# Performance work log

Hardware: AMD Instinct MI355X
Metric: run time of the kernel (lower is better)

## Reference

```python
import jax, jax.numpy as jnp
import numpy as np

K = 7            # pool_size / PSROI_BINS
FEAT_STRIDE = 4
SAMPLES = 2      # bilinear sampling points per bin side (RoIAlign-style avg)


def setup_inputs() -> dict:
    key = jax.random.key(0)
    ks = jax.random.split(key, 4)
    B, H, W, C = 1, 200, 304, 4 * K * K  # C = k*k*dim, dim=4
    features = jax.random.normal(ks[0], (B, H, W, C), jnp.float32)
    Himg, Wimg = H * FEAT_STRIDE, W * FEAT_STRIDE
    N = 512
    u = jax.random.uniform(ks[1], (N, 4), jnp.float32)
    x1 = u[:, 0] * (Wimg - 64.0)
    y1 = u[:, 1] * (Himg - 64.0)
    x2 = jnp.minimum(x1 + 32.0 + u[:, 2] * (Wimg / 4.0), Wimg - 1.0)
    y2 = jnp.minimum(y1 + 32.0 + u[:, 3] * (Himg / 4.0), Himg - 1.0)
    rois = jnp.stack([x1, y1, x2, y2], axis=-1)  # (N,4) image coords
    W_off = jax.random.normal(ks[2], (3, 3, C, 2 * C), jnp.float32) * 0.01
    b_off = jnp.zeros((2 * C,), jnp.float32)
    return {"features": features, "rois": rois, "W_off": W_off, "b_off": b_off}


def _deform_sample(x, off):
    # x: (B,H,W,C); off: (B,H,W,C,2) as (dy,dx) per channel.
    B, H, W, C = x.shape
    gy = jnp.arange(H, dtype=x.dtype)[None, :, None, None]
    gx = jnp.arange(W, dtype=x.dtype)[None, None, :, None]
    yy = jnp.clip(gy + off[..., 0], 0.0, H - 1.0)
    xx = jnp.clip(gx + off[..., 1], 0.0, W - 1.0)
    y0 = jnp.floor(yy); x0 = jnp.floor(xx)
    wy = yy - y0; wx = xx - x0
    y0i = y0.astype(jnp.int32); x0i = x0.astype(jnp.int32)
    y1i = jnp.minimum(y0i + 1, H - 1); x1i = jnp.minimum(x0i + 1, W - 1)
    bi = jnp.arange(B)[:, None, None, None]
    ci = jnp.arange(C)[None, None, None, :]
    v00 = x[bi, y0i, x0i, ci]; v01 = x[bi, y0i, x1i, ci]
    v10 = x[bi, y1i, x0i, ci]; v11 = x[bi, y1i, x1i, ci]
    top = v00 + (v01 - v00) * wx
    bot = v10 + (v11 - v10) * wx
    return top + (bot - top) * wy


def _ps_roi(fm, rois):
    # fm: (H,W,C) offset feature map; rois: (N,4) image coords (x1,y1,x2,y2).
    H, W, C = fm.shape
    dim = C // (K * K)
    fmg = fm.reshape(H, W, K * K, dim)  # position-sensitive channel groups
    b = rois / jnp.asarray(FEAT_STRIDE, fm.dtype)
    x1, y1, x2, y2 = b[:, 0], b[:, 1], b[:, 2], b[:, 3]
    bh = (y2 - y1) / K; bw = (x2 - x1) / K  # per-roi bin sizes (N,)
    i = jnp.arange(K, dtype=fm.dtype)
    s = (jnp.arange(SAMPLES, dtype=fm.dtype) + 0.5) / SAMPLES
    sy = y1[:, None, None] + (i[None, :, None] + s[None, None, :]) * bh[:, None, None]
    sx = x1[:, None, None] + (i[None, :, None] + s[None, None, :]) * bw[:, None, None]
    yy = jnp.clip(sy, 0.0, H - 1.0)[:, :, None, :, None]  # (N,Ki,1,S,1)
    xx = jnp.clip(sx, 0.0, W - 1.0)[:, None, :, None, :]  # (N,1,Kj,1,S)
    y0 = jnp.floor(yy); wy = (yy - y0)[..., None]
    x0 = jnp.floor(xx); wx = (xx - x0)[..., None]
    y0i = y0.astype(jnp.int32); y1i = jnp.minimum(y0i + 1, H - 1)
    x0i = x0.astype(jnp.int32); x1i = jnp.minimum(x0i + 1, W - 1)
    g = (jnp.arange(K)[:, None] * K + jnp.arange(K)[None, :])[None, :, :, None, None]
    v00 = fmg[y0i, x0i, g, :]; v01 = fmg[y0i, x1i, g, :]  # (N,K,K,S,S,dim)
    v10 = fmg[y1i, x0i, g, :]; v11 = fmg[y1i, x1i, g, :]
    top = v00 + (v01 - v00) * wx
    bot = v10 + (v11 - v10) * wx
    vals = top + (bot - top) * wy
    return vals.mean(axis=(3, 4))  # (N,K,K,dim)


def reference(features, rois, W_off, b_off):
    B, H, W, C = features.shape
    offs = jax.lax.conv_general_dilated(
        features, W_off, (1, 1), "SAME",
        dimension_numbers=("NHWC", "HWIO", "NHWC")) + b_off  # (B,H,W,2C)
    off = offs.reshape(B, H, W, C, 2)
    offset_map = _deform_sample(features, off)  # deformable offset resampling
    return _ps_roi(offset_map[0], rois)
```

## Files before the change

kernel.cpp:

```cpp
#include <hip/hip_runtime.h>


constexpr int H = 200, W = 304, C = 196, CO = 392;
constexpr int KK = 7, DIM = 4, NROI = 512;
constexpr int KP = 232;
constexpr int KW = 224;
constexpr size_t WS_NEED = (size_t)49 * 9 * 8 * KW * 2;

typedef __attribute__((ext_vector_type(8))) short bf16x8;
typedef __attribute__((ext_vector_type(4))) float f32x4;

static __device__ inline unsigned short f2bf(float x) {
  unsigned int u = __float_as_uint(x);
  return (unsigned short)((u + 0x7FFFu + ((u >> 16) & 1u)) >> 16);
}

static __device__ inline void roi_geom(const float* __restrict__ rois, int n,
                                       int bi, int bj,
                                       int* ycand, int* xcand,
                                       float* wy, float* wx) {
  const float rx1 = rois[n * 4 + 0] * 0.25f;
  const float ry1 = rois[n * 4 + 1] * 0.25f;
  const float rx2 = rois[n * 4 + 2] * 0.25f;
  const float ry2 = rois[n * 4 + 3] * 0.25f;
  const float bh = (ry2 - ry1) * (1.0f / 7.0f);
  const float bw = (rx2 - rx1) * (1.0f / 7.0f);
#pragma unroll
  for (int si = 0; si < 2; ++si) {
    float sy = ry1 + ((float)bi + ((float)si + 0.5f) * 0.5f) * bh;
    sy = fminf(fmaxf(sy, 0.0f), (float)(H - 1));
    float fy = floorf(sy);
    wy[si] = sy - fy;
    int i0 = (int)fy;
    ycand[2 * si] = i0;
    ycand[2 * si + 1] = min(i0 + 1, H - 1);

    float sx = rx1 + ((float)bj + ((float)si + 0.5f) * 0.5f) * bw;
    sx = fminf(fmaxf(sx, 0.0f), (float)(W - 1));
    float fx = floorf(sx);
    wx[si] = sx - fx;
    int j0 = (int)fx;
    xcand[2 * si] = j0;
    xcand[2 * si + 1] = min(j0 + 1, W - 1);
  }
}

__global__ __launch_bounds__(256) void wprep_kernel(
    const float* __restrict__ Woff, unsigned short* __restrict__ wsb)
{
  const int u = blockIdx.x * 256 + threadIdx.x;
  const int TOT = 49 * 9 * 8 * (KW / 4);
  if (u >= TOT) return;
  const int k4 = u % (KW / 4);
  const int n  = (u / (KW / 4)) % 8;
  const int p  = (u / (KW / 4 * 8)) % 9;
  const int g  = u / (KW / 4 * 8 * 9);
  const int k  = k4 * 4;
  ushort4 v = make_ushort4(0, 0, 0, 0);
  const int o = g * 8 + n;
#pragma unroll
  for (int j = 0; j < 4; ++j) {
    if (k + j < C) {
      const float w = Woff[(size_t)(p * C + k + j) * CO + o];
      ((unsigned short*)&v)[j] = f2bf(w);
    }
  }
  *reinterpret_cast<ushort4*>(wsb + ((size_t)(g * 9 + p) * 8 + n) * KW + k) = v;
}

template <bool USE_WS>
__global__ __launch_bounds__(256) void psroi_union_kernel(
    const float* __restrict__ feat, const float* __restrict__ rois,
    const unsigned short* __restrict__ wsb, const float* __restrict__ Woff,
    const float* __restrict__ boff, float* __restrict__ out)
{
  const int bid = blockIdx.x;
  const int wid = (bid & 7) * (49 * NROI / 8) + (bid >> 3);
  const int g = wid % 49;
  const int n = wid / 49;
  const int bi = g / KK, bj = g % KK;
  const int tid = threadIdx.x;
  const int lane = tid & 63;
  const int wv = tid >> 6;
  const int m_lane = lane & 15;
  const int k_hi = lane >> 4;

  __shared__ short Abuf[64 * KP];
  __shared__ float Cbuf[4 * 16 * 9];

  for (int i = tid; i < 64 * (KP - C); i += 256) {
    const int row = i / (KP - C), col = C + i % (KP - C);
    Abuf[row * KP + col] = 0;
  }

  int yc4[4], xc4[4];
  float wy2[2], wx2[2];
  roi_geom(rois, n, bi, bj, yc4, xc4, wy2, wx2);

  {
    const int pos = tid >> 2;
    const int yi = pos >> 3, xi = pos & 7;
    const int yrow = (yi < 4) ? (yc4[0] + yi - 1) : (yc4[2] + yi - 5);
    const int xcol = (xi < 4) ? (xc4[0] + xi - 1) : (xc4[2] + xi - 5);
    const bool valid = (yrow >= 0) && (yrow < H) && (xcol >= 0) && (xcol < W);
    const float* frow = feat + (size_t)(yrow * W + xcol) * C;
    short* arow = &Abuf[pos * KP];
    const int l = tid & 3;
#pragma unroll
    for (int k = 0; k <= 12; ++k) {
      const int c = l + 4 * k;
      if (c < 49) {
        ushort4 v = make_ushort4(0, 0, 0, 0);
        if (valid) {
          const float4 f4 = *reinterpret_cast<const float4*>(frow + 4 * c);
          v.x = f2bf(f4.x); v.y = f2bf(f4.y);
          v.z = f2bf(f4.z); v.w = f2bf(f4.w);
        }
        *reinterpret_cast<ushort4*>(arow + 4 * c) = v;
      }
    }
  }
  __syncthreads();

  const int i0 = m_lane >> 2, j0 = m_lane & 3;
  const int dyA = yc4[1] - yc4[0], dyB = yc4[3] - yc4[2];
  const int dxA = xc4[1] - xc4[0], dxB = xc4[3] - xc4[2];
  int ybase = (i0 & 2) ? 5 : 1;
  ybase += (i0 & 1) ? ((i0 & 2) ? dyB : dyA) : 0;
  int xbase = (j0 & 2) ? 5 : 1;
  xbase += (j0 & 1) ? ((j0 & 2) ? dxB : dxA) : 0;

  f32x4 acc = {0.f, 0.f, 0.f, 0.f};

#pragma unroll 1
  for (int p = wv; p < 9; p += 4) {
    bf16x8 bfr[7];
#pragma unroll
    for (int ks = 0; ks < 7; ++ks) bfr[ks] = (bf16x8)(short)0;
    if (m_lane < 8) {
      if (USE_WS) {
        const unsigned short* wrow =
            wsb + ((size_t)(g * 9 + p) * 8 + m_lane) * KW + k_hi * 8;
#pragma unroll
        for (int ks = 0; ks < 7; ++ks)
          bfr[ks] = *reinterpret_cast<const bf16x8*>(wrow + ks * 32);
      } else {
#pragma unroll
        for (int ks = 0; ks < 7; ++ks) {
          bf16x8 b = (bf16x8)(short)0;
#pragma unroll
          for (int j = 0; j < 8; ++j) {
            const int k = ks * 32 + k_hi * 8 + j;
            if (k < C)
              b[j] = (short)f2bf(Woff[(size_t)(p * C + k) * CO + g * 8 + m_lane]);
          }
          bfr[ks] = b;
        }
      }
    }

    const int row = (ybase + p / 3 - 1) * 8 + (xbase + p % 3 - 1);
    const short* arow = &Abuf[row * KP];
#pragma unroll
    for (int ks = 0; ks < 7; ++ks) {
      const bf16x8 a = *reinterpret_cast<const bf16x8*>(arow + ks * 32 + k_hi * 8);
      acc = __builtin_amdgcn_mfma_f32_16x16x32_bf16(a, bfr[ks], acc, 0, 0, 0);
    }
  }

  if (m_lane < 8) {
#pragma unroll
    for (int r = 0; r < 4; ++r)
      Cbuf[(wv * 16 + k_hi * 4 + r) * 9 + m_lane] = acc[r];
  }
  __syncthreads();

  if (tid < 64) {
    const int corner = tid >> 2;
    const int d = tid & 3;
    const int yc = yc4[corner >> 2];
    const int xc = xc4[corner & 3];
    const int c = g * DIM + d;

    float offy = boff[2 * c], offx = boff[2 * c + 1];
#pragma unroll
    for (int w = 0; w < 4; ++w) {
      offy += Cbuf[(w * 16 + corner) * 9 + 2 * d];
      offx += Cbuf[(w * 16 + corner) * 9 + 2 * d + 1];
    }

    float yy = fminf(fmaxf((float)yc + offy, 0.0f), (float)(H - 1));
    float xx = fminf(fmaxf((float)xc + offx, 0.0f), (float)(W - 1));
    const float fy = floorf(yy), fx = floorf(xx);
    const float ay = yy - fy, ax = xx - fx;
    const int iy0 = (int)fy, ix0 = (int)fx;
    const int iy1 = min(iy0 + 1, H - 1), ix1 = min(ix0 + 1, W - 1);
    const float v00 = feat[(size_t)(iy0 * W + ix0) * C + c];
    const float v01 = feat[(size_t)(iy0 * W + ix1) * C + c];
    const float v10 = feat[(size_t)(iy1 * W + ix0) * C + c];
    const float v11 = feat[(size_t)(iy1 * W + ix1) * C + c];
    const float top = v00 + (v01 - v00) * ax;
    const float bot = v10 + (v11 - v10) * ax;
    const float om = top + (bot - top) * ay;

    const int yci = corner >> 2, xci = corner & 3;
    const int si = yci >> 1, a = yci & 1;
    const int sj = xci >> 1, b = xci & 1;
    const float cy = a ? wy2[si] : 1.0f - wy2[si];
    const float cx = b ? wx2[sj] : 1.0f - wx2[sj];
    float v = 0.25f * cy * cx * om;

    v += __shfl_xor(v, 4);
    v += __shfl_xor(v, 8);
    v += __shfl_xor(v, 16);
    v += __shfl_xor(v, 32);

    if (tid < 4)
      out[(size_t)n * (KK * KK * DIM) + g * DIM + tid] = v;
  }
}

extern "C" void kernel_launch(void* const* d_in, const int* in_sizes, int n_in,
                              void* d_out, int out_size, void* d_ws, size_t ws_size,
                              hipStream_t stream) {
  const float* feat = (const float*)d_in[0];
  const float* rois = (const float*)d_in[1];
  const float* Woff = (const float*)d_in[2];
  const float* boff = (const float*)d_in[3];
  float* out = (float*)d_out;
  unsigned short* wsb = (unsigned short*)d_ws;

  const int nblocks = 49 * NROI;
  if (ws_size >= WS_NEED) {
    const int prep_tot = 49 * 9 * 8 * (KW / 4);
    wprep_kernel<<<dim3((prep_tot + 255) / 256), dim3(256), 0, stream>>>(Woff, wsb);
    psroi_union_kernel<true><<<dim3(nblocks), dim3(256), 0, stream>>>(
        feat, rois, wsb, Woff, boff, out);
  } else {
    psroi_union_kernel<false><<<dim3(nblocks), dim3(256), 0, stream>>>(
        feat, rois, wsb, Woff, boff, out);
  }
}
```

Before: 208.8 us.

## Pre-convert feature map to padded bf16 and compute one site per wave

Adds a prep kernel that converts the whole feature map to a channel-padded bf16 copy in workspace. A new direct kernel then has each wave handle one (roi, bin) site, loading MFMA A and B operands straight from global bf16 buffers. This removes the per-block LDS staging, fp32-to-bf16 conversion and reduction across waves, and cuts the block count by four. In exchange it needs a much larger workspace and adds a full-map conversion pass; the old kernel stays as the fallback when workspace is too small.

```diff
diff --git a/kernel.cpp b/kernel.cpp
--- a/kernel.cpp
+++ b/kernel.cpp
@@ -3,9 +3,11 @@
 
 constexpr int H = 200, W = 304, C = 196, CO = 392;
 constexpr int KK = 7, DIM = 4, NROI = 512;
+constexpr int KW = 224;
 constexpr int KP = 232;
-constexpr int KW = 224;
-constexpr size_t WS_NEED = (size_t)49 * 9 * 8 * KW * 2;
+constexpr size_t F_ELEMS = (size_t)H * W * KW;
+constexpr size_t W_ELEMS = (size_t)49 * 9 * 8 * KW;
+constexpr size_t WS_NEED = (F_ELEMS + W_ELEMS) * 2;
 
 typedef __attribute__((ext_vector_type(8))) short bf16x8;
 typedef __attribute__((ext_vector_type(4))) float f32x4;
@@ -45,8 +47,25 @@
   }
 }
 
+__global__ __launch_bounds__(256) void fprep_kernel(
+    const float* __restrict__ feat, unsigned short* __restrict__ fbf)
+{
+  const long long u = (long long)blockIdx.x * 256 + threadIdx.x;
+  const long long TOT = (long long)H * W * (KW / 4);
+  if (u >= TOT) return;
+  const int k4 = (int)(u % (KW / 4));
+  const long long pix = u / (KW / 4);
+  const int k = k4 * 4;
+  ushort4 v = make_ushort4(0, 0, 0, 0);
+  const float* src = feat + pix * C;
+#pragma unroll
+  for (int j = 0; j < 4; ++j)
+    if (k + j < C) ((unsigned short*)&v)[j] = f2bf(src[k + j]);
+  *reinterpret_cast<ushort4*>(fbf + pix * KW + k) = v;
+}
+
 __global__ __launch_bounds__(256) void wprep_kernel(
-    const float* __restrict__ Woff, unsigned short* __restrict__ wsb)
+    const float* __restrict__ Woff, unsigned short* __restrict__ wbf)
 {
   const int u = blockIdx.x * 256 + threadIdx.x;
   const int TOT = 49 * 9 * 8 * (KW / 4);
@@ -59,135 +78,74 @@
   ushort4 v = make_ushort4(0, 0, 0, 0);
   const int o = g * 8 + n;
 #pragma unroll
-  for (int j = 0; j < 4; ++j) {
-    if (k + j < C) {
-      const float w = Woff[(size_t)(p * C + k + j) * CO + o];
-      ((unsigned short*)&v)[j] = f2bf(w);
-    }
-  }
-  *reinterpret_cast<ushort4*>(wsb + ((size_t)(g * 9 + p) * 8 + n) * KW + k) = v;
-}
-
-template <bool USE_WS>
-__global__ __launch_bounds__(256) void psroi_union_kernel(
+  for (int j = 0; j < 4; ++j)
+    if (k + j < C)
+      ((unsigned short*)&v)[j] = f2bf(Woff[(size_t)(p * C + k + j) * CO + o]);
+  *reinterpret_cast<ushort4*>(wbf + ((size_t)(g * 9 + p) * 8 + n) * KW + k) = v;
+}
+
+__global__ __launch_bounds__(256) void psroi_direct_kernel(
     const float* __restrict__ feat, const float* __restrict__ rois,
-    const unsigned short* __restrict__ wsb, const float* __restrict__ Woff,
+    const unsigned short* __restrict__ fbf,
+    const unsigned short* __restrict__ wbf,
     const float* __restrict__ boff, float* __restrict__ out)
 {
   const int bid = blockIdx.x;
-  const int wid = (bid & 7) * (49 * NROI / 8) + (bid >> 3);
-  const int g = wid % 49;
-  const int n = wid / 49;
+  const int wid = (bid & 7) * (49 * NROI / 4 / 8) + (bid >> 3);
+  const int wv = threadIdx.x >> 6;
+  const int lane = threadIdx.x & 63;
+  const int site = wid * 4 + wv;
+  const int n = site / 49, g = site % 49;
   const int bi = g / KK, bj = g % KK;
-  const int tid = threadIdx.x;
-  const int lane = tid & 63;
-  const int wv = tid >> 6;
   const int m_lane = lane & 15;
   const int k_hi = lane >> 4;
 
-  __shared__ short Abuf[64 * KP];
-  __shared__ float Cbuf[4 * 16 * 9];
-
-  for (int i = tid; i < 64 * (KP - C); i += 256) {
-    const int row = i / (KP - C), col = C + i % (KP - C);
-    Abuf[row * KP + col] = 0;
-  }
+  __shared__ float Cw[4][16][9];
 
   int yc4[4], xc4[4];
   float wy2[2], wx2[2];
   roi_geom(rois, n, bi, bj, yc4, xc4, wy2, wx2);
 
+  const int ycc = yc4[m_lane >> 2];
+  const int xcc = xc4[m_lane & 3];
+
+  f32x4 acc = {0.f, 0.f, 0.f, 0.f};
+
+#pragma unroll 1
+  for (int p = 0; p < 9; ++p) {
+    const int dy = p / 3 - 1, dx = p % 3 - 1;
+    const int ys = ycc + dy, xs = xcc + dx;
+    const bool valid = (ys >= 0) && (ys < H) && (xs >= 0) && (xs < W);
+    const unsigned short* arow = fbf + (size_t)(ys * W + xs) * KW + k_hi * 8;
+    const unsigned short* brow =
+        wbf + ((size_t)(g * 9 + p) * 8 + m_lane) * KW + k_hi * 8;
+    const bool bval = (m_lane < 8);
+#pragma unroll
+    for (int ks = 0; ks < 7; ++ks) {
+      bf16x8 a = (bf16x8)(short)0;
+      if (valid) a = *reinterpret_cast<const bf16x8*>(arow + ks * 32);
+      bf16x8 b = (bf16x8)(short)0;
+      if (bval) b = *reinterpret_cast<const bf16x8*>(brow + ks * 32);
+      acc = __builtin_amdgcn_mfma_f32_16x16x32_bf16(a, b, acc, 0, 0, 0);
+    }
+  }
+
+  if (m_lane < 8) {
+#pragma unroll
+    for (int r = 0; r < 4; ++r)
+      Cw[wv][k_hi * 4 + r][m_lane] = acc[r];
+  }
+  __syncthreads();
+
   {
-    const int pos = tid >> 2;
-    const int yi = pos >> 3, xi = pos & 7;
-    const int yrow = (yi < 4) ? (yc4[0] + yi - 1) : (yc4[2] + yi - 5);
-    const int xcol = (xi < 4) ? (xc4[0] + xi - 1) : (xc4[2] + xi - 5);
-    const bool valid = (yrow >= 0) && (yrow < H) && (xcol >= 0) && (xcol < W);
-    const float* frow = feat + (size_t)(yrow * W + xcol) * C;
-    short* arow = &Abuf[pos * KP];
-    const int l = tid & 3;
-#pragma unroll
-    for (int k = 0; k <= 12; ++k) {
-      const int c = l + 4 * k;
-      if (c < 49) {
-        ushort4 v = make_ushort4(0, 0, 0, 0);
-        if (valid) {
-          const float4 f4 = *reinterpret_cast<const float4*>(frow + 4 * c);
-          v.x = f2bf(f4.x); v.y = f2bf(f4.y);
-          v.z = f2bf(f4.z); v.w = f2bf(f4.w);
-        }
-        *reinterpret_cast<ushort4*>(arow + 4 * c) = v;
-      }
-    }
-  }
-  __syncthreads();
-
-  const int i0 = m_lane >> 2, j0 = m_lane & 3;
-  const int dyA = yc4[1] - yc4[0], dyB = yc4[3] - yc4[2];
-  const int dxA = xc4[1] - xc4[0], dxB = xc4[3] - xc4[2];
-  int ybase = (i0 & 2) ? 5 : 1;
-  ybase += (i0 & 1) ? ((i0 & 2) ? dyB : dyA) : 0;
-  int xbase = (j0 & 2) ? 5 : 1;
-  xbase += (j0 & 1) ? ((j0 & 2) ? dxB : dxA) : 0;
-
-  f32x4 acc = {0.f, 0.f, 0.f, 0.f};
-
-#pragma unroll 1
-  for (int p = wv; p < 9; p += 4) {
-    bf16x8 bfr[7];
-#pragma unroll
-    for (int ks = 0; ks < 7; ++ks) bfr[ks] = (bf16x8)(short)0;
-    if (m_lane < 8) {
-      if (USE_WS) {
-        const unsigned short* wrow =
-            wsb + ((size_t)(g * 9 + p) * 8 + m_lane) * KW + k_hi * 8;
-#pragma unroll
-        for (int ks = 0; ks < 7; ++ks)
-          bfr[ks] = *reinterpret_cast<const bf16x8*>(wrow + ks * 32);
-      } else {
-#pragma unroll
-        for (int ks = 0; ks < 7; ++ks) {
-          bf16x8 b = (bf16x8)(short)0;
-#pragma unroll
-          for (int j = 0; j < 8; ++j) {
-            const int k = ks * 32 + k_hi * 8 + j;
-            if (k < C)
-              b[j] = (short)f2bf(Woff[(size_t)(p * C + k) * CO + g * 8 + m_lane]);
-          }
-          bfr[ks] = b;
-        }
-      }
-    }
-
-    const int row = (ybase + p / 3 - 1) * 8 + (xbase + p % 3 - 1);
-    const short* arow = &Abuf[row * KP];
-#pragma unroll
-    for (int ks = 0; ks < 7; ++ks) {
-      const bf16x8 a = *reinterpret_cast<const bf16x8*>(arow + ks * 32 + k_hi * 8);
-      acc = __builtin_amdgcn_mfma_f32_16x16x32_bf16(a, bfr[ks], acc, 0, 0, 0);
-    }
-  }
-
-  if (m_lane < 8) {
-#pragma unroll
-    for (int r = 0; r < 4; ++r)
-      Cbuf[(wv * 16 + k_hi * 4 + r) * 9 + m_lane] = acc[r];
-  }
-  __syncthreads();
-
-  if (tid < 64) {
-    const int corner = tid >> 2;
-    const int d = tid & 3;
+    const int corner = lane >> 2;
+    const int d = lane & 3;
     const int yc = yc4[corner >> 2];
     const int xc = xc4[corner & 3];
     const int c = g * DIM + d;
 
-    float offy = boff[2 * c], offx = boff[2 * c + 1];
-#pragma unroll
-    for (int w = 0; w < 4; ++w) {
-      offy += Cbuf[(w * 16 + corner) * 9 + 2 * d];
-      offx += Cbuf[(w * 16 + corner) * 9 + 2 * d + 1];
-    }
+    const float offy = Cw[wv][corner][2 * d]     + boff[2 * c];
+    const float offx = Cw[wv][corner][2 * d + 1] + boff[2 * c + 1];
 
     float yy = fminf(fmaxf((float)yc + offy, 0.0f), (float)(H - 1));
     float xx = fminf(fmaxf((float)xc + offx, 0.0f), (float)(W - 1));
@@ -215,6 +173,148 @@
     v += __shfl_xor(v, 16);
     v += __shfl_xor(v, 32);
 
+    if (lane < 4)
+      out[(size_t)n * (KK * KK * DIM) + g * DIM + lane] = v;
+  }
+}
+
+__global__ __launch_bounds__(256) void psroi_union_kernel(
+    const float* __restrict__ feat, const float* __restrict__ rois,
+    const float* __restrict__ Woff, const float* __restrict__ boff,
+    float* __restrict__ out)
+{
+  const int bid = blockIdx.x;
+  const int wid = (bid & 7) * (49 * NROI / 8) + (bid >> 3);
+  const int g = wid % 49;
+  const int n = wid / 49;
+  const int bi = g / KK, bj = g % KK;
+  const int tid = threadIdx.x;
+  const int lane = tid & 63;
+  const int wv = tid >> 6;
+  const int m_lane = lane & 15;
+  const int k_hi = lane >> 4;
+
+  __shared__ short Abuf[64 * KP];
+  __shared__ float Cbuf[4 * 16 * 9];
+
+  for (int i = tid; i < 64 * (KP - C); i += 256) {
+    const int row = i / (KP - C), col = C + i % (KP - C);
+    Abuf[row * KP + col] = 0;
+  }
+
+  int yc4[4], xc4[4];
+  float wy2[2], wx2[2];
+  roi_geom(rois, n, bi, bj, yc4, xc4, wy2, wx2);
+
+  {
+    const int pos = tid >> 2;
+    const int yi = pos >> 3, xi = pos & 7;
+    const int yrow = (yi < 4) ? (yc4[0] + yi - 1) : (yc4[2] + yi - 5);
+    const int xcol = (xi < 4) ? (xc4[0] + xi - 1) : (xc4[2] + xi - 5);
+    const bool valid = (yrow >= 0) && (yrow < H) && (xcol >= 0) && (xcol < W);
+    const float* frow = feat + (size_t)(yrow * W + xcol) * C;
+    short* arow = &Abuf[pos * KP];
+    const int l = tid & 3;
+#pragma unroll
+    for (int k = 0; k <= 12; ++k) {
+      const int c = l + 4 * k;
+      if (c < 49) {
+        ushort4 v = make_ushort4(0, 0, 0, 0);
+        if (valid) {
+          const float4 f4 = *reinterpret_cast<const float4*>(frow + 4 * c);
+          v.x = f2bf(f4.x); v.y = f2bf(f4.y);
+          v.z = f2bf(f4.z); v.w = f2bf(f4.w);
+        }
+        *reinterpret_cast<ushort4*>(arow + 4 * c) = v;
+      }
+    }
+  }
+  __syncthreads();
+
+  const int i0 = m_lane >> 2, j0 = m_lane & 3;
+  const int dyA = yc4[1] - yc4[0], dyB = yc4[3] - yc4[2];
+  const int dxA = xc4[1] - xc4[0], dxB = xc4[3] - xc4[2];
+  int ybase = (i0 & 2) ? 5 : 1;
+  ybase += (i0 & 1) ? ((i0 & 2) ? dyB : dyA) : 0;
+  int xbase = (j0 & 2) ? 5 : 1;
+  xbase += (j0 & 1) ? ((j0 & 2) ? dxB : dxA) : 0;
+
+  f32x4 acc = {0.f, 0.f, 0.f, 0.f};
+
+#pragma unroll 1
+  for (int p = wv; p < 9; p += 4) {
+    bf16x8 bfr[7];
+#pragma unroll
+    for (int ks = 0; ks < 7; ++ks) bfr[ks] = (bf16x8)(short)0;
+    if (m_lane < 8) {
+#pragma unroll
+      for (int ks = 0; ks < 7; ++ks) {
+        bf16x8 b = (bf16x8)(short)0;
+#pragma unroll
+        for (int j = 0; j < 8; ++j) {
+          const int k = ks * 32 + k_hi * 8 + j;
+          if (k < C)
+            b[j] = (short)f2bf(Woff[(size_t)(p * C + k) * CO + g * 8 + m_lane]);
+        }
+        bfr[ks] = b;
+      }
+    }
+    const int row = (ybase + p / 3 - 1) * 8 + (xbase + p % 3 - 1);
+    const short* arow = &Abuf[row * KP];
+#pragma unroll
+    for (int ks = 0; ks < 7; ++ks) {
+      const bf16x8 a = *reinterpret_cast<const bf16x8*>(arow + ks * 32 + k_hi * 8);
+      acc = __builtin_amdgcn_mfma_f32_16x16x32_bf16(a, bfr[ks], acc, 0, 0, 0);
+    }
+  }
+
+  if (m_lane < 8) {
+#pragma unroll
+    for (int r = 0; r < 4; ++r)
+      Cbuf[(wv * 16 + k_hi * 4 + r) * 9 + m_lane] = acc[r];
+  }
+  __syncthreads();
+
+  if (tid < 64) {
+    const int corner = tid >> 2;
+    const int d = tid & 3;
+    const int yc = yc4[corner >> 2];
+    const int xc = xc4[corner & 3];
+    const int c = g * DIM + d;
+
+    float offy = boff[2 * c], offx = boff[2 * c + 1];
+#pragma unroll
+    for (int w = 0; w < 4; ++w) {
+      offy += Cbuf[(w * 16 + corner) * 9 + 2 * d];
+      offx += Cbuf[(w * 16 + corner) * 9 + 2 * d + 1];
+    }
+
+    float yy = fminf(fmaxf((float)yc + offy, 0.0f), (float)(H - 1));
+    float xx = fminf(fmaxf((float)xc + offx, 0.0f), (float)(W - 1));
+    const float fy = floorf(yy), fx = floorf(xx);
+    const float ay = yy - fy, ax = xx - fx;
+    const int iy0 = (int)fy, ix0 = (int)fx;
+    const int iy1 = min(iy0 + 1, H - 1), ix1 = min(ix0 + 1, W - 1);
+    const float v00 = feat[(size_t)(iy0 * W + ix0) * C + c];
+    const float v01 = feat[(size_t)(iy0 * W + ix1) * C + c];
+    const float v10 = feat[(size_t)(iy1 * W + ix0) * C + c];
+    const float v11 = feat[(size_t)(iy1 * W + ix1) * C + c];
+    const float top = v00 + (v01 - v00) * ax;
+    const float bot = v10 + (v11 - v10) * ax;
+    const float om = top + (bot - top) * ay;
+
+    const int yci = corner >> 2, xci = corner & 3;
+    const int si = yci >> 1, a = yci & 1;
+    const int sj = xci >> 1, b = xci & 1;
+    const float cy = a ? wy2[si] : 1.0f - wy2[si];
+    const float cx = b ? wx2[sj] : 1.0f - wx2[sj];
+    float v = 0.25f * cy * cx * om;
+
+    v += __shfl_xor(v, 4);
+    v += __shfl_xor(v, 8);
+    v += __shfl_xor(v, 16);
+    v += __shfl_xor(v, 32);
+
     if (tid < 4)
       out[(size_t)n * (KK * KK * DIM) + g * DIM + tid] = v;
   }
@@ -228,16 +328,19 @@
   const float* Woff = (const float*)d_in[2];
   const float* boff = (const float*)d_in[3];
   float* out = (float*)d_out;
-  unsigned short* wsb = (unsigned short*)d_ws;
-
-  const int nblocks = 49 * NROI;
+
   if (ws_size >= WS_NEED) {
-    const int prep_tot = 49 * 9 * 8 * (KW / 4);
-    wprep_kernel<<<dim3((prep_tot + 255) / 256), dim3(256), 0, stream>>>(Woff, wsb);
-    psroi_union_kernel<true><<<dim3(nblocks), dim3(256), 0, stream>>>(
-        feat, rois, wsb, Woff, boff, out);
+    unsigned short* fbf = (unsigned short*)d_ws;
+    unsigned short* wbf = fbf + F_ELEMS;
+    const long long ftot = (long long)H * W * (KW / 4);
+    fprep_kernel<<<dim3((unsigned)((ftot + 255) / 256)), dim3(256), 0, stream>>>(
+        feat, fbf);
+    const int wtot = 49 * 9 * 8 * (KW / 4);
+    wprep_kernel<<<dim3((wtot + 255) / 256), dim3(256), 0, stream>>>(Woff, wbf);
+    psroi_direct_kernel<<<dim3(49 * NROI / 4), dim3(256), 0, stream>>>(
+        feat, rois, fbf, wbf, boff, out);
   } else {
-    psroi_union_kernel<false><<<dim3(nblocks), dim3(256), 0, stream>>>(
-        feat, rois, wsb, Woff, boff, out);
-  }
-}
+    psroi_union_kernel<<<dim3(49 * NROI), dim3(256), 0, stream>>>(
+        feat, rois, Woff, boff, out);
+  }
+}
```

New measurement: 240.8 us. 1.15x slower.
